# Kernel optimization log

Hardware: AMD Instinct MI355X
Metric: run time of the kernel (lower is better)

The kernel has to match this reference:

```python
import jax, jax.numpy as jnp
import numpy as np

B, S, D, H = 2, 2048, 1024, 16
HD = D // H
SCALE = HD ** -0.5


def setup_inputs() -> dict:
    key = jax.random.key(0)
    ks = jax.random.split(key, 11)
    std = D ** -0.5
    inp = {
        'query': jax.random.normal(ks[0], (B, S, D), jnp.float32),
        'key': jax.random.normal(ks[1], (B, S, D), jnp.float32),
        'value': jax.random.normal(ks[2], (B, S, D), jnp.float32),
        'Wq': jax.random.normal(ks[3], (D, D), jnp.float32) * std,
        'bq': jnp.zeros((D,), jnp.float32),
        'Wk': jax.random.normal(ks[4], (D, D), jnp.float32) * std,
        'bk': jnp.zeros((D,), jnp.float32),
        'Wv': jax.random.normal(ks[5], (D, D), jnp.float32) * std,
        'bv': jnp.zeros((D,), jnp.float32),
        'Wo': jax.random.normal(ks[6], (D, D), jnp.float32) * std,
        'bo': jnp.zeros((D,), jnp.float32),
    }
    return inp


def reference(query, key, value, Wq, bq, Wk, bk, Wv, bv, Wo, bo):
    # Linear projections (torch Linear: x @ W.T + b), split into heads -> [B,H,S,HD]
    def proj(x, W, b):
        y = jnp.einsum('bsd,ed->bse', x, W) + b
        return y.reshape(B, S, H, HD).transpose(0, 2, 1, 3)

    Q = proj(query, Wq, bq)
    K = proj(key, Wk, bk)
    V = proj(value, Wv, bv)
    scores = jnp.einsum('bhqd,bhkd->bhqk', Q, K) * SCALE  # [B,H,S,S]
    attn = jax.nn.softmax(scores, axis=-1)
    ctx = jnp.einsum('bhqk,bhkd->bhqd', attn, V)
    ctx = ctx.transpose(0, 2, 1, 3).reshape(B, S, D)
    out = jnp.einsum('bsd,ed->bse', ctx, Wo) + bo
    return out
```

## Files before the change

kernel.cpp:

```cpp
#include <hip/hip_runtime.h>
#include <hip/hip_bf16.h>

#define DEVFN __device__ __forceinline__

typedef __attribute__((ext_vector_type(8))) short bf16x8;
typedef __attribute__((ext_vector_type(4))) float f32x4;
typedef __attribute__((ext_vector_type(16))) float f32x16;

constexpr int Bc = 2, Sc = 2048, Dc = 1024, Hc = 16, HDc = 64;
constexpr float SCALEc = 0.125f;
constexpr float LOG2E  = 1.44269504088896340736f;

DEVFN unsigned short f2bf(float f) {
    union { float f; unsigned int u; } x; x.f = f;
    return (unsigned short)((x.u + 0x7fffu + ((x.u >> 16) & 1u)) >> 16);
}

DEVFN f32x4 mfma16(bf16x8 a, bf16x8 b, f32x4 c) {
    return __builtin_amdgcn_mfma_f32_16x16x32_bf16(a, b, c, 0, 0, 0);
}
DEVFN f32x16 mfma32(bf16x8 a, bf16x8 b, f32x16 c) {
    return __builtin_amdgcn_mfma_f32_32x32x16_bf16(a, b, c, 0, 0, 0);
}

DEVFN void gload16(const void* g, void* l) {
    __builtin_amdgcn_global_load_lds((const __attribute__((address_space(1))) void*)g,
                                     (__attribute__((address_space(3))) void*)l, 16, 0, 0);
}

__global__ __launch_bounds__(256) void cvt_all(
    const float* __restrict__ q, const float* __restrict__ k, const float* __restrict__ v,
    const float* __restrict__ wq, const float* __restrict__ wk,
    const float* __restrict__ wv, const float* __restrict__ wo,
    unsigned short* __restrict__ qb, unsigned short* __restrict__ kb, unsigned short* __restrict__ vb,
    unsigned short* __restrict__ wqb, unsigned short* __restrict__ wkb,
    unsigned short* __restrict__ wvb, unsigned short* __restrict__ wob)
{
    const unsigned t = blockIdx.x * 256 + threadIdx.x;
    const float* s; unsigned short* d; unsigned local;
    if (t < (3u << 19)) {
        const unsigned which = t >> 19; local = t & ((1u << 19) - 1);
        s = which == 0 ? q : which == 1 ? k : v;
        d = which == 0 ? qb : which == 1 ? kb : vb;
    } else {
        const unsigned t2 = t - (3u << 19);
        const unsigned which = t2 >> 17; local = t2 & ((1u << 17) - 1);
        s = which == 0 ? wq : which == 1 ? wk : which == 2 ? wv : wo;
        d = which == 0 ? wqb : which == 1 ? wkb : which == 2 ? wvb : wob;
    }
    const size_t off = (size_t)local * 8;
    float4 v0 = *(const float4*)(s + off);
    float4 v1 = *(const float4*)(s + off + 4);
    unsigned short t8[8] = {f2bf(v0.x), f2bf(v0.y), f2bf(v0.z), f2bf(v0.w),
                            f2bf(v1.x), f2bf(v1.y), f2bf(v1.z), f2bf(v1.w)};
    *(uint4*)(d + off) = *(const uint4*)t8;
}

__global__ __launch_bounds__(256) void qkv_gemm(
    const unsigned short* __restrict__ Aq, const unsigned short* __restrict__ Ak,
    const unsigned short* __restrict__ Av,
    const unsigned short* __restrict__ Wqb, const unsigned short* __restrict__ Wkb,
    const unsigned short* __restrict__ Wvb,
    const float* __restrict__ bqp, const float* __restrict__ bkp, const float* __restrict__ bvp,
    unsigned short* __restrict__ Qo, unsigned short* __restrict__ Ko, unsigned short* __restrict__ Vto)
{
    __shared__ short As[2][4096];
    __shared__ short Bs[2][4096];

    const int g = blockIdx.x >> 8;
    const unsigned short* A  = g == 0 ? Aq  : g == 1 ? Ak  : Av;
    const unsigned short* Bw = g == 0 ? Wqb : g == 1 ? Wkb : Wvb;
    const float* bias = g == 0 ? bqp : g == 1 ? bkp : bvp;
    const float scale = g == 0 ? SCALEc * LOG2E : 1.0f;

    const int tid = threadIdx.x, lane = tid & 63, w = tid >> 6;
    const int lr = lane & 15, lg = lane >> 4;
    const int bid = blockIdx.x & 255;
    const int tm = bid & 31, tn = bid >> 5;
    const int wm = (w >> 1) * 64, wn = (w & 1) * 64;

    const int c0 = 2 * w, c1 = 2 * w + 1;
    const int r0 = c0 * 16 + (lane >> 2), r1 = c1 * 16 + (lane >> 2);
    const int sl0 = ((lane & 3) ^ ((r0 >> 1) & 3)) * 8, sl1 = ((lane & 3) ^ ((r1 >> 1) & 3)) * 8;
    const unsigned short* Ap0 = A  + (size_t)(tm * 128 + r0) * 1024 + sl0;
    const unsigned short* Ap1 = A  + (size_t)(tm * 128 + r1) * 1024 + sl1;
    const unsigned short* Bp0 = Bw + (size_t)(tn * 128 + r0) * 1024 + sl0;
    const unsigned short* Bp1 = Bw + (size_t)(tn * 128 + r1) * 1024 + sl1;

    f32x4 acc[4][4] = {};
    const int fread = (lr >> 1) & 3;

    gload16(Ap0, &As[0][c0 * 512]);
    gload16(Ap1, &As[0][c1 * 512]);
    gload16(Bp0, &Bs[0][c0 * 512]);
    gload16(Bp1, &Bs[0][c1 * 512]);

    int cur = 0;
    for (int k0 = 0; k0 < 1024; k0 += 32) {
        const int nk = (k0 + 32 < 1024) ? k0 + 32 : k0;
        gload16(Ap0 + nk, &As[cur ^ 1][c0 * 512]);
        gload16(Ap1 + nk, &As[cur ^ 1][c1 * 512]);
        gload16(Bp0 + nk, &Bs[cur ^ 1][c0 * 512]);
        gload16(Bp1 + nk, &Bs[cur ^ 1][c1 * 512]);
        asm volatile("s_waitcnt vmcnt(4)" ::: "memory");
        __builtin_amdgcn_s_barrier();
        __builtin_amdgcn_sched_barrier(0);

        const short* Ac = As[cur];
        const short* Bc2 = Bs[cur];
        bf16x8 af[4], bfv[4];
        #pragma unroll
        for (int m = 0; m < 4; m++) {
            const int row = wm + m * 16 + lr;
            af[m] = *(const bf16x8*)&Ac[row * 32 + (lg ^ fread) * 8];
        }
        #pragma unroll
        for (int n = 0; n < 4; n++) {
            const int row = wn + n * 16 + lr;
            bfv[n] = *(const bf16x8*)&Bc2[row * 32 + (lg ^ fread) * 8];
        }
        #pragma unroll
        for (int m = 0; m < 4; m++)
            #pragma unroll
            for (int n = 0; n < 4; n++)
                acc[m][n] = mfma16(af[m], bfv[n], acc[m][n]);

        asm volatile("s_waitcnt lgkmcnt(0)" ::: "memory");
        __builtin_amdgcn_sched_barrier(0);
        __builtin_amdgcn_s_barrier();
        cur ^= 1;
    }
    asm volatile("s_waitcnt vmcnt(0)" ::: "memory");

    if (g < 2) {
        unsigned short* Y = g == 0 ? Qo : Ko;
        #pragma unroll
        for (int n = 0; n < 4; n++) {
            const int col = tn * 128 + wn + n * 16 + lr;
            const float bv = bias[col];
            const int hh = col >> 6, hd = col & 63;
            #pragma unroll
            for (int m = 0; m < 4; m++) {
                const int row0 = tm * 128 + wm + m * 16 + lg * 4;
                const int b_ = row0 >> 11, sQ = row0 & 2047;
                #pragma unroll
                for (int r = 0; r < 4; r++) {
                    const float val = (acc[m][n][r] + bv) * scale;
                    Y[(((size_t)(b_ * Hc + hh)) * Sc + (sQ + r)) * HDc + hd] = f2bf(val);
                }
            }
        }
    } else {
        #pragma unroll
        for (int n = 0; n < 4; n++) {
            const int col = tn * 128 + wn + n * 16 + lr;
            const float bv = bias[col];
            const int hh = col >> 6, hd = col & 63;
            #pragma unroll
            for (int m = 0; m < 4; m++) {
                const int row0 = tm * 128 + wm + m * 16 + lg * 4;
                const int b_ = row0 >> 11, sQ = row0 & 2047;
                const int sQp = (sQ & ~12) | ((sQ & 4) << 1) | ((sQ & 8) >> 1);
                unsigned long long pk = 0;
                #pragma unroll
                for (int r = 0; r < 4; r++)
                    pk |= (unsigned long long)f2bf(acc[m][n][r] + bv) << (16 * r);
                *(unsigned long long*)&Vto[(((size_t)(b_ * Hc + hh)) * HDc + hd) * Sc + sQp] = pk;
            }
        }
    }
}

__global__ __launch_bounds__(256) void out_gemm(
    const unsigned short* __restrict__ Ab, const unsigned short* __restrict__ Bw,
    const float* __restrict__ bias, float* __restrict__ Y)
{
    __shared__ short As[2][4096];
    __shared__ short Bs[2][4096];
    const int tid = threadIdx.x, lane = tid & 63, w = tid >> 6;
    const int lr = lane & 15, lg = lane >> 4;
    const int tm = blockIdx.x & 31, tn = blockIdx.x >> 5;
    const int wm = (w >> 1) * 64, wn = (w & 1) * 64;

    const int c0 = 2 * w, c1 = 2 * w + 1;
    const int r0 = c0 * 16 + (lane >> 2), r1 = c1 * 16 + (lane >> 2);
    const int sl0 = ((lane & 3) ^ ((r0 >> 1) & 3)) * 8, sl1 = ((lane & 3) ^ ((r1 >> 1) & 3)) * 8;
    const unsigned short* Ap0 = Ab + (size_t)(tm * 128 + r0) * 1024 + sl0;
    const unsigned short* Ap1 = Ab + (size_t)(tm * 128 + r1) * 1024 + sl1;
    const unsigned short* Bp0 = Bw + (size_t)(tn * 128 + r0) * 1024 + sl0;
    const unsigned short* Bp1 = Bw + (size_t)(tn * 128 + r1) * 1024 + sl1;

    f32x4 acc[4][4] = {};
    const int fread = (lr >> 1) & 3;

    gload16(Ap0, &As[0][c0 * 512]);
    gload16(Ap1, &As[0][c1 * 512]);
    gload16(Bp0, &Bs[0][c0 * 512]);
    gload16(Bp1, &Bs[0][c1 * 512]);

    int cur = 0;
    for (int k0 = 0; k0 < 1024; k0 += 32) {
        const int nk = (k0 + 32 < 1024) ? k0 + 32 : k0;
        gload16(Ap0 + nk, &As[cur ^ 1][c0 * 512]);
        gload16(Ap1 + nk, &As[cur ^ 1][c1 * 512]);
        gload16(Bp0 + nk, &Bs[cur ^ 1][c0 * 512]);
        gload16(Bp1 + nk, &Bs[cur ^ 1][c1 * 512]);
        asm volatile("s_waitcnt vmcnt(4)" ::: "memory");
        __builtin_amdgcn_s_barrier();
        __builtin_amdgcn_sched_barrier(0);

        const short* Ac = As[cur];
        const short* Bc2 = Bs[cur];
        bf16x8 af[4], bfv[4];
        #pragma unroll
        for (int m = 0; m < 4; m++) {
            const int row = wm + m * 16 + lr;
            af[m] = *(const bf16x8*)&Ac[row * 32 + (lg ^ fread) * 8];
        }
        #pragma unroll
        for (int n = 0; n < 4; n++) {
            const int row = wn + n * 16 + lr;
            bfv[n] = *(const bf16x8*)&Bc2[row * 32 + (lg ^ fread) * 8];
        }
        #pragma unroll
        for (int m = 0; m < 4; m++)
            #pragma unroll
            for (int n = 0; n < 4; n++)
                acc[m][n] = mfma16(af[m], bfv[n], acc[m][n]);

        asm volatile("s_waitcnt lgkmcnt(0)" ::: "memory");
        __builtin_amdgcn_sched_barrier(0);
        __builtin_amdgcn_s_barrier();
        cur ^= 1;
    }
    asm volatile("s_waitcnt vmcnt(0)" ::: "memory");

    #pragma unroll
    for (int n = 0; n < 4; n++) {
        const int col = tn * 128 + wn + n * 16 + lr;
        const float bv = bias[col];
        #pragma unroll
        for (int m = 0; m < 4; m++) {
            const int row0 = tm * 128 + wm + m * 16 + lg * 4;
            #pragma unroll
            for (int r = 0; r < 4; r++)
                Y[(size_t)(row0 + r) * 1024 + col] = acc[m][n][r] + bv;
        }
    }
}

__global__ __launch_bounds__(512, 2) void attn_fwd(
    const unsigned short* __restrict__ Q, const unsigned short* __restrict__ Kg,
    const unsigned short* __restrict__ Vtg, unsigned short* __restrict__ ctx)
{
    __shared__ short Ks[2][4096];
    __shared__ short Vs[2][4096];

    const int tid = threadIdx.x, lane = tid & 63, w = tid >> 6;
    const int l31 = lane & 31, hi = lane >> 5;

    const int blk = blockIdx.x;
    const int idx = blk >> 3;
    const int bh = (blk & 7) * 4 + (idx >> 3);
    const int qt = idx & 7;

    const unsigned short* Qb = Q   + (size_t)bh * Sc * HDc;
    const unsigned short* Kb = Kg  + (size_t)bh * Sc * HDc;
    const unsigned short* Vb = Vtg + (size_t)bh * HDc * Sc;

    const int qbase = qt * 256 + w * 32;
    bf16x8 qf[4];
    {
        const size_t qr = (size_t)(qbase + l31) * HDc + hi * 8;
        #pragma unroll
        for (int kk = 0; kk < 4; kk++)
            qf[kk] = *(const bf16x8*)&Qb[qr + kk * 16];
    }

    const int srow  = w * 8 + (lane >> 3);
    const int sslot = ((lane & 7) ^ (lane >> 3)) * 8;
    const unsigned short* Kst = Kb + (size_t)srow * HDc + sslot;
    const unsigned short* Vst = Vb + (size_t)srow * Sc + sslot;

    const int swk = lane & 7;

    const f32x16 Z = {};
    f32x16 acc0 = {}, acc1 = {}, accl = {};

    union { unsigned int u[4]; bf16x8 v; } ones;
    ones.u[0] = ones.u[1] = ones.u[2] = ones.u[3] = 0x3F803F80u;

    gload16(Kst, &Ks[0][w * 512]);
    gload16(Vst, &Vs[0][w * 512]);

    int cur = 0;
    for (int kt = 0; kt < 32; ++kt) {
        {
            const int nxt = kt < 31 ? kt + 1 : 31;
            gload16(Kst + (size_t)nxt * 4096, &Ks[cur ^ 1][w * 512]);
            gload16(Vst + nxt * 64,           &Vs[cur ^ 1][w * 512]);
        }
        asm volatile("s_waitcnt vmcnt(2)" ::: "memory");
        __builtin_amdgcn_s_barrier();
        __builtin_amdgcn_sched_barrier(0);

        const short* Kc = Ks[cur];
        const short* Vc = Vs[cur];

        f32x16 sf0, sf1;
        __builtin_amdgcn_s_setprio(1);
        {
            const int sl = (hi ^ swk) * 8;
            bf16x8 a0 = *(const bf16x8*)&Kc[l31 * 64 + sl];
            bf16x8 a1 = *(const bf16x8*)&Kc[(32 + l31) * 64 + sl];
            sf0 = mfma32(a0, qf[0], Z);
            sf1 = mfma32(a1, qf[0], Z);
        }
        #pragma unroll
        for (int kk = 1; kk < 4; kk++) {
            const int sl = ((2 * kk + hi) ^ swk) * 8;
            bf16x8 a0 = *(const bf16x8*)&Kc[l31 * 64 + sl];
            bf16x8 a1 = *(const bf16x8*)&Kc[(32 + l31) * 64 + sl];
            sf0 = mfma32(a0, qf[kk], sf0);
            sf1 = mfma32(a1, qf[kk], sf1);
        }
        __builtin_amdgcn_s_setprio(0);

        unsigned int p0[8], p1[8];
        #pragma unroll
        for (int j = 0; j < 8; j++) {
            const float a0 = __builtin_amdgcn_exp2f(sf0[2 * j]);
            const float a1 = __builtin_amdgcn_exp2f(sf0[2 * j + 1]);
            const float b0 = __builtin_amdgcn_exp2f(sf1[2 * j]);
            const float b1 = __builtin_amdgcn_exp2f(sf1[2 * j + 1]);
            asm("v_cvt_pk_bf16_f32 %0, %1, %2" : "=v"(p0[j]) : "v"(a0), "v"(a1));
            asm("v_cvt_pk_bf16_f32 %0, %1, %2" : "=v"(p1[j]) : "v"(b0), "v"(b1));
        }

        __builtin_amdgcn_s_setprio(1);
        #pragma unroll
        for (int m = 0; m < 4; m++) {
            const unsigned int* pw = (m < 2) ? &p0[(m & 1) * 4] : &p1[(m & 1) * 4];
            union { unsigned int u[4]; bf16x8 v; } af;
            af.u[0] = pw[0]; af.u[1] = pw[1]; af.u[2] = pw[2]; af.u[3] = pw[3];
            const int sl = ((2 * m + hi) ^ swk) * 8;
            bf16x8 b0 = *(const bf16x8*)&Vc[l31 * 64 + sl];
            bf16x8 b1 = *(const bf16x8*)&Vc[(32 + l31) * 64 + sl];
            acc0 = mfma32(af.v, b0, acc0);
            acc1 = mfma32(af.v, b1, acc1);
            accl = mfma32(af.v, ones.v, accl);
        }
        __builtin_amdgcn_s_setprio(0);

        asm volatile("s_waitcnt lgkmcnt(0)" ::: "memory");
        __builtin_amdgcn_sched_barrier(0);
        __builtin_amdgcn_s_barrier();
        cur ^= 1;
    }
    asm volatile("s_waitcnt vmcnt(0)" ::: "memory");

    const int b_ = bh >> 4, hh = bh & 15;
    #pragma unroll
    for (int r = 0; r < 16; r++) {
        const int qr = (r & 3) + 8 * (r >> 2) + 4 * hi;
        const float lv = __builtin_amdgcn_rcpf(accl[r]);
        const int sq = qbase + qr;
        unsigned short* co = &ctx[((size_t)(b_ * Sc + sq)) * Dc + (size_t)hh * HDc + l31];
        co[0]  = f2bf(acc0[r] * lv);
        co[32] = f2bf(acc1[r] * lv);
    }
}

extern "C" void kernel_launch(void* const* d_in, const int* in_sizes, int n_in,
                              void* d_out, int out_size, void* d_ws, size_t ws_size,
                              hipStream_t stream)
{
    const float* query = (const float*)d_in[0];
    const float* key   = (const float*)d_in[1];
    const float* value = (const float*)d_in[2];
    const float* Wq = (const float*)d_in[3];
    const float* bq = (const float*)d_in[4];
    const float* Wk = (const float*)d_in[5];
    const float* bk = (const float*)d_in[6];
    const float* Wv = (const float*)d_in[7];
    const float* bv = (const float*)d_in[8];
    const float* Wo = (const float*)d_in[9];
    const float* bo = (const float*)d_in[10];

    constexpr size_t W = 1048576, AE = 4194304;
    unsigned short* wqb = (unsigned short*)d_ws;
    unsigned short* wkb = wqb + W;
    unsigned short* wvb = wkb + W;
    unsigned short* wob = wvb + W;
    unsigned short* qb  = wob + W;
    unsigned short* kb  = qb + AE;
    unsigned short* vb  = kb + AE;
    unsigned short* Qh  = vb + AE;
    unsigned short* Kh  = Qh + AE;
    unsigned short* Vth = Kh + AE;
    unsigned short* cx  = qb;

    cvt_all<<<8192, 256, 0, stream>>>(query, key, value, Wq, Wk, Wv, Wo,
                                      qb, kb, vb, wqb, wkb, wvb, wob);
    qkv_gemm<<<768, 256, 0, stream>>>(qb, kb, vb, wqb, wkb, wvb,
                                      bq, bk, bv, Qh, Kh, Vth);
    attn_fwd<<<256, 512, 0, stream>>>(Qh, Kh, Vth, cx);
    out_gemm<<<256, 256, 0, stream>>>(cx, wob, bo, (float*)d_out);
}
```

Measured before the change: 131.0 us.

## Triple-buffer GEMM K-tiles and split attention into smaller 4-wave blocks

Both projection GEMMs move from double to triple-buffered LDS staging, prefetching two K-tiles ahead and waiting on vmcnt(8), so global load latency is better hidden behind MFMA work. The attention kernel goes from 256 blocks of 8 waves to 512 blocks of 4 waves. Each wave now loads twice as many K/V staging rows, and the block-to-(head, q-tile) mapping is adjusted to match. This adds LDS use per GEMM block and doubles per-block K/V load traffic in attention, in exchange for more deeply pipelined GEMMs and finer attention scheduling across CUs.

```diff
diff --git a/kernel.cpp b/kernel.cpp
--- a/kernel.cpp
+++ b/kernel.cpp
@@ -64,8 +64,8 @@
     const float* __restrict__ bqp, const float* __restrict__ bkp, const float* __restrict__ bvp,
     unsigned short* __restrict__ Qo, unsigned short* __restrict__ Ko, unsigned short* __restrict__ Vto)
 {
-    __shared__ short As[2][4096];
-    __shared__ short Bs[2][4096];
+    __shared__ short As[3 * 4096];
+    __shared__ short Bs[3 * 4096];
 
     const int g = blockIdx.x >> 8;
     const unsigned short* A  = g == 0 ? Aq  : g == 1 ? Ak  : Av;
@@ -90,24 +90,28 @@
     f32x4 acc[4][4] = {};
     const int fread = (lr >> 1) & 3;
 
-    gload16(Ap0, &As[0][c0 * 512]);
-    gload16(Ap1, &As[0][c1 * 512]);
-    gload16(Bp0, &Bs[0][c0 * 512]);
-    gload16(Bp1, &Bs[0][c1 * 512]);
-
-    int cur = 0;
+    gload16(Ap0,      As + 0    + c0 * 512);
+    gload16(Ap1,      As + 0    + c1 * 512);
+    gload16(Bp0,      Bs + 0    + c0 * 512);
+    gload16(Bp1,      Bs + 0    + c1 * 512);
+    gload16(Ap0 + 32, As + 4096 + c0 * 512);
+    gload16(Ap1 + 32, As + 4096 + c1 * 512);
+    gload16(Bp0 + 32, Bs + 4096 + c0 * 512);
+    gload16(Bp1 + 32, Bs + 4096 + c1 * 512);
+
+    int bR = 0, bN1 = 4096, bN2 = 8192;
     for (int k0 = 0; k0 < 1024; k0 += 32) {
-        const int nk = (k0 + 32 < 1024) ? k0 + 32 : k0;
-        gload16(Ap0 + nk, &As[cur ^ 1][c0 * 512]);
-        gload16(Ap1 + nk, &As[cur ^ 1][c1 * 512]);
-        gload16(Bp0 + nk, &Bs[cur ^ 1][c0 * 512]);
-        gload16(Bp1 + nk, &Bs[cur ^ 1][c1 * 512]);
-        asm volatile("s_waitcnt vmcnt(4)" ::: "memory");
-        __builtin_amdgcn_s_barrier();
-        __builtin_amdgcn_sched_barrier(0);
-
-        const short* Ac = As[cur];
-        const short* Bc2 = Bs[cur];
+        const int nk = (k0 + 64 < 1024) ? k0 + 64 : 992;
+        gload16(Ap0 + nk, As + bN2 + c0 * 512);
+        gload16(Ap1 + nk, As + bN2 + c1 * 512);
+        gload16(Bp0 + nk, Bs + bN2 + c0 * 512);
+        gload16(Bp1 + nk, Bs + bN2 + c1 * 512);
+        asm volatile("s_waitcnt vmcnt(8)" ::: "memory");
+        __builtin_amdgcn_s_barrier();
+        __builtin_amdgcn_sched_barrier(0);
+
+        const short* Ac  = As + bR;
+        const short* Bc2 = Bs + bR;
         bf16x8 af[4], bfv[4];
         #pragma unroll
         for (int m = 0; m < 4; m++) {
@@ -128,7 +132,7 @@
         asm volatile("s_waitcnt lgkmcnt(0)" ::: "memory");
         __builtin_amdgcn_sched_barrier(0);
         __builtin_amdgcn_s_barrier();
-        cur ^= 1;
+        const int t = bR; bR = bN1; bN1 = bN2; bN2 = t;
     }
     asm volatile("s_waitcnt vmcnt(0)" ::: "memory");
 
@@ -175,8 +179,8 @@
     const unsigned short* __restrict__ Ab, const unsigned short* __restrict__ Bw,
     const float* __restrict__ bias, float* __restrict__ Y)
 {
-    __shared__ short As[2][4096];
-    __shared__ short Bs[2][4096];
+    __shared__ short As[3 * 4096];
+    __shared__ short Bs[3 * 4096];
     const int tid = threadIdx.x, lane = tid & 63, w = tid >> 6;
     const int lr = lane & 15, lg = lane >> 4;
     const int tm = blockIdx.x & 31, tn = blockIdx.x >> 5;
@@ -193,24 +197,28 @@
     f32x4 acc[4][4] = {};
     const int fread = (lr >> 1) & 3;
 
-    gload16(Ap0, &As[0][c0 * 512]);
-    gload16(Ap1, &As[0][c1 * 512]);
-    gload16(Bp0, &Bs[0][c0 * 512]);
-    gload16(Bp1, &Bs[0][c1 * 512]);
-
-    int cur = 0;
+    gload16(Ap0,      As + 0    + c0 * 512);
+    gload16(Ap1,      As + 0    + c1 * 512);
+    gload16(Bp0,      Bs + 0    + c0 * 512);
+    gload16(Bp1,      Bs + 0    + c1 * 512);
+    gload16(Ap0 + 32, As + 4096 + c0 * 512);
+    gload16(Ap1 + 32, As + 4096 + c1 * 512);
+    gload16(Bp0 + 32, Bs + 4096 + c0 * 512);
+    gload16(Bp1 + 32, Bs + 4096 + c1 * 512);
+
+    int bR = 0, bN1 = 4096, bN2 = 8192;
     for (int k0 = 0; k0 < 1024; k0 += 32) {
-        const int nk = (k0 + 32 < 1024) ? k0 + 32 : k0;
-        gload16(Ap0 + nk, &As[cur ^ 1][c0 * 512]);
-        gload16(Ap1 + nk, &As[cur ^ 1][c1 * 512]);
-        gload16(Bp0 + nk, &Bs[cur ^ 1][c0 * 512]);
-        gload16(Bp1 + nk, &Bs[cur ^ 1][c1 * 512]);
-        asm volatile("s_waitcnt vmcnt(4)" ::: "memory");
-        __builtin_amdgcn_s_barrier();
-        __builtin_amdgcn_sched_barrier(0);
-
-        const short* Ac = As[cur];
-        const short* Bc2 = Bs[cur];
+        const int nk = (k0 + 64 < 1024) ? k0 + 64 : 992;
+        gload16(Ap0 + nk, As + bN2 + c0 * 512);
+        gload16(Ap1 + nk, As + bN2 + c1 * 512);
+        gload16(Bp0 + nk, Bs + bN2 + c0 * 512);
+        gload16(Bp1 + nk, Bs + bN2 + c1 * 512);
+        asm volatile("s_waitcnt vmcnt(8)" ::: "memory");
+        __builtin_amdgcn_s_barrier();
+        __builtin_amdgcn_sched_barrier(0);
+
+        const short* Ac  = As + bR;
+        const short* Bc2 = Bs + bR;
         bf16x8 af[4], bfv[4];
         #pragma unroll
         for (int m = 0; m < 4; m++) {
@@ -231,7 +239,7 @@
         asm volatile("s_waitcnt lgkmcnt(0)" ::: "memory");
         __builtin_amdgcn_sched_barrier(0);
         __builtin_amdgcn_s_barrier();
-        cur ^= 1;
+        const int t = bR; bR = bN1; bN1 = bN2; bN2 = t;
     }
     asm volatile("s_waitcnt vmcnt(0)" ::: "memory");
 
@@ -249,7 +257,7 @@
     }
 }
 
-__global__ __launch_bounds__(512, 2) void attn_fwd(
+__global__ __launch_bounds__(256) void attn_fwd(
     const unsigned short* __restrict__ Q, const unsigned short* __restrict__ Kg,
     const unsigned short* __restrict__ Vtg, unsigned short* __restrict__ ctx)
 {
@@ -261,14 +269,14 @@
 
     const int blk = blockIdx.x;
     const int idx = blk >> 3;
-    const int bh = (blk & 7) * 4 + (idx >> 3);
-    const int qt = idx & 7;
+    const int bh = (blk & 7) * 4 + (idx >> 4);
+    const int qt = idx & 15;
 
     const unsigned short* Qb = Q   + (size_t)bh * Sc * HDc;
     const unsigned short* Kb = Kg  + (size_t)bh * Sc * HDc;
     const unsigned short* Vb = Vtg + (size_t)bh * HDc * Sc;
 
-    const int qbase = qt * 256 + w * 32;
+    const int qbase = qt * 128 + w * 32;
     bf16x8 qf[4];
     {
         const size_t qr = (size_t)(qbase + l31) * HDc + hi * 8;
@@ -277,7 +285,7 @@
             qf[kk] = *(const bf16x8*)&Qb[qr + kk * 16];
     }
 
-    const int srow  = w * 8 + (lane >> 3);
+    const int srow  = w * 16 + (lane >> 3);
     const int sslot = ((lane & 7) ^ (lane >> 3)) * 8;
     const unsigned short* Kst = Kb + (size_t)srow * HDc + sslot;
     const unsigned short* Vst = Vb + (size_t)srow * Sc + sslot;
@@ -290,17 +298,25 @@
     union { unsigned int u[4]; bf16x8 v; } ones;
     ones.u[0] = ones.u[1] = ones.u[2] = ones.u[3] = 0x3F803F80u;
 
-    gload16(Kst, &Ks[0][w * 512]);
-    gload16(Vst, &Vs[0][w * 512]);
+    gload16(Kst,          &Ks[0][w * 1024]);
+    gload16(Kst + 512,    &Ks[0][w * 1024 + 512]);
+    gload16(Vst,          &Vs[0][w * 1024]);
+    gload16(Vst + 8 * Sc, &Vs[0][w * 1024 + 512]);
 
     int cur = 0;
     for (int kt = 0; kt < 32; ++kt) {
         {
             const int nxt = kt < 31 ? kt + 1 : 31;
-            gload16(Kst + (size_t)nxt * 4096, &Ks[cur ^ 1][w * 512]);
-            gload16(Vst + nxt * 64,           &Vs[cur ^ 1][w * 512]);
-        }
-        asm volatile("s_waitcnt vmcnt(2)" ::: "memory");
+            const unsigned short* kp = Kst + (size_t)nxt * 4096;
+            const unsigned short* vp = Vst + nxt * 64;
+            short* kl = &Ks[cur ^ 1][w * 1024];
+            short* vl = &Vs[cur ^ 1][w * 1024];
+            gload16(kp,           kl);
+            gload16(kp + 512,     kl + 512);
+            gload16(vp,           vl);
+            gload16(vp + 8 * Sc,  vl + 512);
+        }
+        asm volatile("s_waitcnt vmcnt(4)" ::: "memory");
         __builtin_amdgcn_s_barrier();
         __builtin_amdgcn_sched_barrier(0);
 
@@ -404,6 +420,6 @@
                                       qb, kb, vb, wqb, wkb, wvb, wob);
     qkv_gemm<<<768, 256, 0, stream>>>(qb, kb, vb, wqb, wkb, wvb,
                                       bq, bk, bv, Qh, Kh, Vth);
-    attn_fwd<<<256, 512, 0, stream>>>(Qh, Kh, Vth, cx);
+    attn_fwd<<<512, 256, 0, stream>>>(Qh, Kh, Vth, cx);
     out_gemm<<<256, 256, 0, stream>>>(cx, wob, bo, (float*)d_out);
 }
```

Result: slower. 136.2 us (+3.9%).

## Fuse fp32-to-bf16 activation conversion into QKV GEMM A-tile loads

Applied to the files above, without the earlier changes.

Stops the separate pass that converts query/key/value to bf16 into a workspace. The QKV GEMM now loads fp32 activation rows straight into registers two k-steps ahead, converts them with packed bf16 conversion instructions, and writes them into the swizzled LDS tile, while weights still arrive via direct global-to-LDS loads. This removes a full read/write round trip of the activations and part of a kernel launch. In exchange the GEMM reads twice the A bytes per tile, needs more registers for the in-flight loads (launch bounds set to 3 waves), and puts conversion ALU work inside the main loop.

```diff
diff --git a/kernel.cpp b/kernel.cpp
--- a/kernel.cpp
+++ b/kernel.cpp
@@ -28,26 +28,16 @@
                                      (__attribute__((address_space(3))) void*)l, 16, 0, 0);
 }
 
-__global__ __launch_bounds__(256) void cvt_all(
-    const float* __restrict__ q, const float* __restrict__ k, const float* __restrict__ v,
+__global__ __launch_bounds__(256) void cvt_w(
     const float* __restrict__ wq, const float* __restrict__ wk,
     const float* __restrict__ wv, const float* __restrict__ wo,
-    unsigned short* __restrict__ qb, unsigned short* __restrict__ kb, unsigned short* __restrict__ vb,
     unsigned short* __restrict__ wqb, unsigned short* __restrict__ wkb,
     unsigned short* __restrict__ wvb, unsigned short* __restrict__ wob)
 {
     const unsigned t = blockIdx.x * 256 + threadIdx.x;
-    const float* s; unsigned short* d; unsigned local;
-    if (t < (3u << 19)) {
-        const unsigned which = t >> 19; local = t & ((1u << 19) - 1);
-        s = which == 0 ? q : which == 1 ? k : v;
-        d = which == 0 ? qb : which == 1 ? kb : vb;
-    } else {
-        const unsigned t2 = t - (3u << 19);
-        const unsigned which = t2 >> 17; local = t2 & ((1u << 17) - 1);
-        s = which == 0 ? wq : which == 1 ? wk : which == 2 ? wv : wo;
-        d = which == 0 ? wqb : which == 1 ? wkb : which == 2 ? wvb : wob;
-    }
+    const unsigned which = t >> 17, local = t & ((1u << 17) - 1);
+    const float* s = which == 0 ? wq : which == 1 ? wk : which == 2 ? wv : wo;
+    unsigned short* d = which == 0 ? wqb : which == 1 ? wkb : which == 2 ? wvb : wob;
     const size_t off = (size_t)local * 8;
     float4 v0 = *(const float4*)(s + off);
     float4 v1 = *(const float4*)(s + off + 4);
@@ -56,9 +46,8 @@
     *(uint4*)(d + off) = *(const uint4*)t8;
 }
 
-__global__ __launch_bounds__(256) void qkv_gemm(
-    const unsigned short* __restrict__ Aq, const unsigned short* __restrict__ Ak,
-    const unsigned short* __restrict__ Av,
+__global__ __launch_bounds__(256, 3) void qkv_gemm(
+    const float* __restrict__ Aq, const float* __restrict__ Ak, const float* __restrict__ Av,
     const unsigned short* __restrict__ Wqb, const unsigned short* __restrict__ Wkb,
     const unsigned short* __restrict__ Wvb,
     const float* __restrict__ bqp, const float* __restrict__ bkp, const float* __restrict__ bvp,
@@ -68,7 +57,7 @@
     __shared__ short Bs[2][4096];
 
     const int g = blockIdx.x >> 8;
-    const unsigned short* A  = g == 0 ? Aq  : g == 1 ? Ak  : Av;
+    const float* A = g == 0 ? Aq : g == 1 ? Ak : Av;
     const unsigned short* Bw = g == 0 ? Wqb : g == 1 ? Wkb : Wvb;
     const float* bias = g == 0 ? bqp : g == 1 ? bkp : bvp;
     const float scale = g == 0 ? SCALEc * LOG2E : 1.0f;
@@ -81,56 +70,93 @@
 
     const int c0 = 2 * w, c1 = 2 * w + 1;
     const int r0 = c0 * 16 + (lane >> 2), r1 = c1 * 16 + (lane >> 2);
-    const int sl0 = ((lane & 3) ^ ((r0 >> 1) & 3)) * 8, sl1 = ((lane & 3) ^ ((r1 >> 1) & 3)) * 8;
-    const unsigned short* Ap0 = A  + (size_t)(tm * 128 + r0) * 1024 + sl0;
-    const unsigned short* Ap1 = A  + (size_t)(tm * 128 + r1) * 1024 + sl1;
-    const unsigned short* Bp0 = Bw + (size_t)(tn * 128 + r0) * 1024 + sl0;
-    const unsigned short* Bp1 = Bw + (size_t)(tn * 128 + r1) * 1024 + sl1;
+    const int s0 = (lane & 3) ^ ((r0 >> 1) & 3), s1 = (lane & 3) ^ ((r1 >> 1) & 3);
+    const float* Afp0 = A + (size_t)(tm * 128 + r0) * 1024 + s0 * 8;
+    const float* Afp1 = A + (size_t)(tm * 128 + r1) * 1024 + s1 * 8;
+    const unsigned short* Bp0 = Bw + (size_t)(tn * 128 + r0) * 1024 + s0 * 8;
+    const unsigned short* Bp1 = Bw + (size_t)(tn * 128 + r1) * 1024 + s1 * 8;
+    short* AW0[2] = {&As[0][c0 * 512 + lane * 8], &As[1][c0 * 512 + lane * 8]};
+    short* AW1[2] = {&As[0][c1 * 512 + lane * 8], &As[1][c1 * 512 + lane * 8]};
 
     f32x4 acc[4][4] = {};
     const int fread = (lr >> 1) & 3;
 
-    gload16(Ap0, &As[0][c0 * 512]);
-    gload16(Ap1, &As[0][c1 * 512]);
+    float4 fE[4], fO[4];
+
+    fE[0] = *(const float4*)(Afp0);     fE[1] = *(const float4*)(Afp0 + 4);
+    fE[2] = *(const float4*)(Afp1);     fE[3] = *(const float4*)(Afp1 + 4);
     gload16(Bp0, &Bs[0][c0 * 512]);
     gload16(Bp1, &Bs[0][c1 * 512]);
-
-    int cur = 0;
-    for (int k0 = 0; k0 < 1024; k0 += 32) {
-        const int nk = (k0 + 32 < 1024) ? k0 + 32 : k0;
-        gload16(Ap0 + nk, &As[cur ^ 1][c0 * 512]);
-        gload16(Ap1 + nk, &As[cur ^ 1][c1 * 512]);
-        gload16(Bp0 + nk, &Bs[cur ^ 1][c0 * 512]);
-        gload16(Bp1 + nk, &Bs[cur ^ 1][c1 * 512]);
-        asm volatile("s_waitcnt vmcnt(4)" ::: "memory");
-        __builtin_amdgcn_s_barrier();
-        __builtin_amdgcn_sched_barrier(0);
-
-        const short* Ac = As[cur];
-        const short* Bc2 = Bs[cur];
-        bf16x8 af[4], bfv[4];
-        #pragma unroll
-        for (int m = 0; m < 4; m++) {
-            const int row = wm + m * 16 + lr;
-            af[m] = *(const bf16x8*)&Ac[row * 32 + (lg ^ fread) * 8];
-        }
-        #pragma unroll
-        for (int n = 0; n < 4; n++) {
-            const int row = wn + n * 16 + lr;
-            bfv[n] = *(const bf16x8*)&Bc2[row * 32 + (lg ^ fread) * 8];
-        }
-        #pragma unroll
-        for (int m = 0; m < 4; m++)
-            #pragma unroll
-            for (int n = 0; n < 4; n++)
-                acc[m][n] = mfma16(af[m], bfv[n], acc[m][n]);
-
-        asm volatile("s_waitcnt lgkmcnt(0)" ::: "memory");
-        __builtin_amdgcn_sched_barrier(0);
-        __builtin_amdgcn_s_barrier();
-        cur ^= 1;
+    {
+        unsigned int q0, q1, q2, q3;
+        asm("v_cvt_pk_bf16_f32 %0,%1,%2" : "=v"(q0) : "v"(fE[0].x), "v"(fE[0].y));
+        asm("v_cvt_pk_bf16_f32 %0,%1,%2" : "=v"(q1) : "v"(fE[0].z), "v"(fE[0].w));
+        asm("v_cvt_pk_bf16_f32 %0,%1,%2" : "=v"(q2) : "v"(fE[1].x), "v"(fE[1].y));
+        asm("v_cvt_pk_bf16_f32 %0,%1,%2" : "=v"(q3) : "v"(fE[1].z), "v"(fE[1].w));
+        *(uint4*)AW0[0] = (uint4){q0, q1, q2, q3};
+        asm("v_cvt_pk_bf16_f32 %0,%1,%2" : "=v"(q0) : "v"(fE[2].x), "v"(fE[2].y));
+        asm("v_cvt_pk_bf16_f32 %0,%1,%2" : "=v"(q1) : "v"(fE[2].z), "v"(fE[2].w));
+        asm("v_cvt_pk_bf16_f32 %0,%1,%2" : "=v"(q2) : "v"(fE[3].x), "v"(fE[3].y));
+        asm("v_cvt_pk_bf16_f32 %0,%1,%2" : "=v"(q3) : "v"(fE[3].z), "v"(fE[3].w));
+        *(uint4*)AW1[0] = (uint4){q0, q1, q2, q3};
+    }
+    fO[0] = *(const float4*)(Afp0 + 32); fO[1] = *(const float4*)(Afp0 + 36);
+    fO[2] = *(const float4*)(Afp1 + 32); fO[3] = *(const float4*)(Afp1 + 36);
+    asm volatile("s_waitcnt lgkmcnt(0)" ::: "memory");
+
+#define QKV_STEP(KT, P, FI, FC)                                                  \
+    {                                                                            \
+        const int k1 = ((KT) < 31) ? ((KT) + 1) * 32 : 992;                      \
+        const int k2 = ((KT) < 30) ? ((KT) + 2) * 32 : 992;                      \
+        gload16(Bp0 + k1, &Bs[(P) ^ 1][c0 * 512]);                               \
+        gload16(Bp1 + k1, &Bs[(P) ^ 1][c1 * 512]);                               \
+        FI[0] = *(const float4*)(Afp0 + k2); FI[1] = *(const float4*)(Afp0 + k2 + 4); \
+        FI[2] = *(const float4*)(Afp1 + k2); FI[3] = *(const float4*)(Afp1 + k2 + 4); \
+        asm volatile("s_waitcnt vmcnt(10)" ::: "memory");                        \
+        __builtin_amdgcn_s_barrier();                                            \
+        __builtin_amdgcn_sched_barrier(0);                                       \
+        const short* Ac  = As[P];                                                \
+        const short* Bc2 = Bs[P];                                                \
+        bf16x8 af[4], bfv[4];                                                    \
+        _Pragma("unroll")                                                        \
+        for (int m = 0; m < 4; m++) {                                            \
+            const int row = wm + m * 16 + lr;                                    \
+            af[m] = *(const bf16x8*)&Ac[row * 32 + (lg ^ fread) * 8];            \
+        }                                                                        \
+        _Pragma("unroll")                                                        \
+        for (int n = 0; n < 4; n++) {                                            \
+            const int row = wn + n * 16 + lr;                                    \
+            bfv[n] = *(const bf16x8*)&Bc2[row * 32 + (lg ^ fread) * 8];          \
+        }                                                                        \
+        _Pragma("unroll")                                                        \
+        for (int m = 0; m < 4; m++)                                              \
+            _Pragma("unroll")                                                    \
+            for (int n = 0; n < 4; n++)                                          \
+                acc[m][n] = mfma16(af[m], bfv[n], acc[m][n]);                    \
+        {                                                                        \
+            unsigned int q0, q1, q2, q3;                                         \
+            asm("v_cvt_pk_bf16_f32 %0,%1,%2" : "=v"(q0) : "v"(FC[0].x), "v"(FC[0].y)); \
+            asm("v_cvt_pk_bf16_f32 %0,%1,%2" : "=v"(q1) : "v"(FC[0].z), "v"(FC[0].w)); \
+            asm("v_cvt_pk_bf16_f32 %0,%1,%2" : "=v"(q2) : "v"(FC[1].x), "v"(FC[1].y)); \
+            asm("v_cvt_pk_bf16_f32 %0,%1,%2" : "=v"(q3) : "v"(FC[1].z), "v"(FC[1].w)); \
+            *(uint4*)AW0[(P) ^ 1] = (uint4){q0, q1, q2, q3};                     \
+            asm("v_cvt_pk_bf16_f32 %0,%1,%2" : "=v"(q0) : "v"(FC[2].x), "v"(FC[2].y)); \
+            asm("v_cvt_pk_bf16_f32 %0,%1,%2" : "=v"(q1) : "v"(FC[2].z), "v"(FC[2].w)); \
+            asm("v_cvt_pk_bf16_f32 %0,%1,%2" : "=v"(q2) : "v"(FC[3].x), "v"(FC[3].y)); \
+            asm("v_cvt_pk_bf16_f32 %0,%1,%2" : "=v"(q3) : "v"(FC[3].z), "v"(FC[3].w)); \
+            *(uint4*)AW1[(P) ^ 1] = (uint4){q0, q1, q2, q3};                     \
+        }                                                                        \
+        asm volatile("s_waitcnt lgkmcnt(0)" ::: "memory");                       \
+        __builtin_amdgcn_sched_barrier(0);                                       \
+        __builtin_amdgcn_s_barrier();                                            \
+    }
+
+    for (int kt = 0; kt < 32; kt += 2) {
+        QKV_STEP(kt,     0, fE, fO)
+        QKV_STEP(kt + 1, 1, fO, fE)
     }
     asm volatile("s_waitcnt vmcnt(0)" ::: "memory");
+#undef QKV_STEP
 
     if (g < 2) {
         unsigned short* Y = g == 0 ? Qo : Ko;
@@ -209,7 +235,7 @@
         __builtin_amdgcn_s_barrier();
         __builtin_amdgcn_sched_barrier(0);
 
-        const short* Ac = As[cur];
+        const short* Ac  = As[cur];
         const short* Bc2 = Bs[cur];
         bf16x8 af[4], bfv[4];
         #pragma unroll
@@ -392,17 +418,13 @@
     unsigned short* wkb = wqb + W;
     unsigned short* wvb = wkb + W;
     unsigned short* wob = wvb + W;
-    unsigned short* qb  = wob + W;
-    unsigned short* kb  = qb + AE;
-    unsigned short* vb  = kb + AE;
-    unsigned short* Qh  = vb + AE;
+    unsigned short* Qh  = wob + W;
     unsigned short* Kh  = Qh + AE;
     unsigned short* Vth = Kh + AE;
-    unsigned short* cx  = qb;
-
-    cvt_all<<<8192, 256, 0, stream>>>(query, key, value, Wq, Wk, Wv, Wo,
-                                      qb, kb, vb, wqb, wkb, wvb, wob);
-    qkv_gemm<<<768, 256, 0, stream>>>(qb, kb, vb, wqb, wkb, wvb,
+    unsigned short* cx  = Vth + AE;
+
+    cvt_w<<<2048, 256, 0, stream>>>(Wq, Wk, Wv, Wo, wqb, wkb, wvb, wob);
+    qkv_gemm<<<768, 256, 0, stream>>>(query, key, value, wqb, wkb, wvb,
                                       bq, bk, bv, Qh, Kh, Vth);
     attn_fwd<<<256, 512, 0, stream>>>(Qh, Kh, Vth, cx);
     out_gemm<<<256, 256, 0, stream>>>(cx, wob, bo, (float*)d_out);
```

Measured after the change: 115.5 us. 11.8% less time.

## Fuse fp32-to-bf16 activation conversion into QKV GEMM with larger tiles

Applied to the files above, without the earlier changes.

The separate conversion pass over query/key/value is removed. The QKV GEMM now loads fp32 activations directly, converts them in registers with packed bf16 conversion instructions, and writes them into swizzled LDS. The GEMM also moves to 256x256 tiles with 512 threads, a BK of 64, an XCD-aware block remap and raised wave priority around the MFMA section. This avoids writing and re-reading about 24MB of bf16 activations, in exchange for more fp32 global traffic inside the GEMM and only 192 blocks, which may underfill the device.

```diff
diff --git a/kernel.cpp b/kernel.cpp
--- a/kernel.cpp
+++ b/kernel.cpp
@@ -28,26 +28,16 @@
                                      (__attribute__((address_space(3))) void*)l, 16, 0, 0);
 }
 
-__global__ __launch_bounds__(256) void cvt_all(
-    const float* __restrict__ q, const float* __restrict__ k, const float* __restrict__ v,
+__global__ __launch_bounds__(256) void cvt_w(
     const float* __restrict__ wq, const float* __restrict__ wk,
     const float* __restrict__ wv, const float* __restrict__ wo,
-    unsigned short* __restrict__ qb, unsigned short* __restrict__ kb, unsigned short* __restrict__ vb,
     unsigned short* __restrict__ wqb, unsigned short* __restrict__ wkb,
     unsigned short* __restrict__ wvb, unsigned short* __restrict__ wob)
 {
     const unsigned t = blockIdx.x * 256 + threadIdx.x;
-    const float* s; unsigned short* d; unsigned local;
-    if (t < (3u << 19)) {
-        const unsigned which = t >> 19; local = t & ((1u << 19) - 1);
-        s = which == 0 ? q : which == 1 ? k : v;
-        d = which == 0 ? qb : which == 1 ? kb : vb;
-    } else {
-        const unsigned t2 = t - (3u << 19);
-        const unsigned which = t2 >> 17; local = t2 & ((1u << 17) - 1);
-        s = which == 0 ? wq : which == 1 ? wk : which == 2 ? wv : wo;
-        d = which == 0 ? wqb : which == 1 ? wkb : which == 2 ? wvb : wob;
-    }
+    const unsigned which = t >> 17, local = t & ((1u << 17) - 1);
+    const float* s = which == 0 ? wq : which == 1 ? wk : which == 2 ? wv : wo;
+    unsigned short* d = which == 0 ? wqb : which == 1 ? wkb : which == 2 ? wvb : wob;
     const size_t off = (size_t)local * 8;
     float4 v0 = *(const float4*)(s + off);
     float4 v1 = *(const float4*)(s + off + 4);
@@ -56,34 +46,187 @@
     *(uint4*)(d + off) = *(const uint4*)t8;
 }
 
-__global__ __launch_bounds__(256) void qkv_gemm(
-    const unsigned short* __restrict__ Aq, const unsigned short* __restrict__ Ak,
-    const unsigned short* __restrict__ Av,
+__global__ __launch_bounds__(512, 2) void qkv_gemm(
+    const float* __restrict__ Aq, const float* __restrict__ Ak, const float* __restrict__ Av,
     const unsigned short* __restrict__ Wqb, const unsigned short* __restrict__ Wkb,
     const unsigned short* __restrict__ Wvb,
     const float* __restrict__ bqp, const float* __restrict__ bkp, const float* __restrict__ bvp,
     unsigned short* __restrict__ Qo, unsigned short* __restrict__ Ko, unsigned short* __restrict__ Vto)
 {
-    __shared__ short As[2][4096];
-    __shared__ short Bs[2][4096];
-
-    const int g = blockIdx.x >> 8;
-    const unsigned short* A  = g == 0 ? Aq  : g == 1 ? Ak  : Av;
+    __shared__ short As[2 * 16384];
+    __shared__ short Bs[2 * 16384];
+
+    const int lgid = (blockIdx.x & 7) * 24 + (blockIdx.x >> 3);
+    const int g = lgid >> 6;
+    const int rr = lgid & 63;
+    const int tm = rr >> 2, tn = rr & 3;
+
+    const float* A = g == 0 ? Aq : g == 1 ? Ak : Av;
     const unsigned short* Bw = g == 0 ? Wqb : g == 1 ? Wkb : Wvb;
     const float* bias = g == 0 ? bqp : g == 1 ? bkp : bvp;
     const float scale = g == 0 ? SCALEc * LOG2E : 1.0f;
 
     const int tid = threadIdx.x, lane = tid & 63, w = tid >> 6;
+    const int lr = lane & 15, lgq = lane >> 4;
+    const int wm = (w >> 2) * 128, wn = (w & 3) * 64;
+
+    const int ra = tid >> 1, kh = tid & 1;
+    const int swzra = (ra & 7) ^ (((ra >> 3) & 1) << 2);
+    const float* Ap = A + (size_t)(tm * 256 + ra) * 1024 + kh * 32;
+    const int aw0 = ra * 64 + (((kh * 4 + 0) ^ swzra) * 8);
+    const int aw1 = ra * 64 + (((kh * 4 + 1) ^ swzra) * 8);
+    const int aw2 = ra * 64 + (((kh * 4 + 2) ^ swzra) * 8);
+    const int aw3 = ra * 64 + (((kh * 4 + 3) ^ swzra) * 8);
+
+    const int l3 = lane >> 3, l7 = lane & 7;
+    const unsigned short* Bp[4];
+    #pragma unroll
+    for (int i = 0; i < 4; i++) {
+        const int rb = w * 32 + i * 8 + l3;
+        const int swzrb = (rb & 7) ^ (((rb >> 3) & 1) << 2);
+        Bp[i] = Bw + (size_t)(tn * 256 + rb) * 1024 + ((l7 ^ swzrb) * 8);
+    }
+    const int bdst = (w * 32) * 64;
+
+    const int swzL = (lr & 7) ^ (((lr >> 3) & 1) << 2);
+
+    f32x4 acc[8][4] = {};
+    float4 fA0, fA1, fA2, fA3, fA4, fA5, fA6, fA7;
+
+#define LOAD_A(KO)                                                               \
+    fA0 = *(const float4*)(Ap + (KO));      fA1 = *(const float4*)(Ap + (KO) + 4);  \
+    fA2 = *(const float4*)(Ap + (KO) + 8);  fA3 = *(const float4*)(Ap + (KO) + 12); \
+    fA4 = *(const float4*)(Ap + (KO) + 16); fA5 = *(const float4*)(Ap + (KO) + 20); \
+    fA6 = *(const float4*)(Ap + (KO) + 24); fA7 = *(const float4*)(Ap + (KO) + 28);
+
+#define CVT_A(BUFOFS)                                                            \
+    {                                                                            \
+        unsigned int q0, q1, q2, q3;                                             \
+        asm("v_cvt_pk_bf16_f32 %0,%1,%2" : "=v"(q0) : "v"(fA0.x), "v"(fA0.y));   \
+        asm("v_cvt_pk_bf16_f32 %0,%1,%2" : "=v"(q1) : "v"(fA0.z), "v"(fA0.w));   \
+        asm("v_cvt_pk_bf16_f32 %0,%1,%2" : "=v"(q2) : "v"(fA1.x), "v"(fA1.y));   \
+        asm("v_cvt_pk_bf16_f32 %0,%1,%2" : "=v"(q3) : "v"(fA1.z), "v"(fA1.w));   \
+        *(uint4*)&As[(BUFOFS) + aw0] = (uint4){q0, q1, q2, q3};                  \
+        asm("v_cvt_pk_bf16_f32 %0,%1,%2" : "=v"(q0) : "v"(fA2.x), "v"(fA2.y));   \
+        asm("v_cvt_pk_bf16_f32 %0,%1,%2" : "=v"(q1) : "v"(fA2.z), "v"(fA2.w));   \
+        asm("v_cvt_pk_bf16_f32 %0,%1,%2" : "=v"(q2) : "v"(fA3.x), "v"(fA3.y));   \
+        asm("v_cvt_pk_bf16_f32 %0,%1,%2" : "=v"(q3) : "v"(fA3.z), "v"(fA3.w));   \
+        *(uint4*)&As[(BUFOFS) + aw1] = (uint4){q0, q1, q2, q3};                  \
+        asm("v_cvt_pk_bf16_f32 %0,%1,%2" : "=v"(q0) : "v"(fA4.x), "v"(fA4.y));   \
+        asm("v_cvt_pk_bf16_f32 %0,%1,%2" : "=v"(q1) : "v"(fA4.z), "v"(fA4.w));   \
+        asm("v_cvt_pk_bf16_f32 %0,%1,%2" : "=v"(q2) : "v"(fA5.x), "v"(fA5.y));   \
+        asm("v_cvt_pk_bf16_f32 %0,%1,%2" : "=v"(q3) : "v"(fA5.z), "v"(fA5.w));   \
+        *(uint4*)&As[(BUFOFS) + aw2] = (uint4){q0, q1, q2, q3};                  \
+        asm("v_cvt_pk_bf16_f32 %0,%1,%2" : "=v"(q0) : "v"(fA6.x), "v"(fA6.y));   \
+        asm("v_cvt_pk_bf16_f32 %0,%1,%2" : "=v"(q1) : "v"(fA6.z), "v"(fA6.w));   \
+        asm("v_cvt_pk_bf16_f32 %0,%1,%2" : "=v"(q2) : "v"(fA7.x), "v"(fA7.y));   \
+        asm("v_cvt_pk_bf16_f32 %0,%1,%2" : "=v"(q3) : "v"(fA7.z), "v"(fA7.w));   \
+        *(uint4*)&As[(BUFOFS) + aw3] = (uint4){q0, q1, q2, q3};                  \
+    }
+
+    gload16(Bp[0], &Bs[bdst + 0]);
+    gload16(Bp[1], &Bs[bdst + 512]);
+    gload16(Bp[2], &Bs[bdst + 1024]);
+    gload16(Bp[3], &Bs[bdst + 1536]);
+    LOAD_A(0)
+    CVT_A(0)
+    asm volatile("s_waitcnt vmcnt(0) lgkmcnt(0)" ::: "memory");
+    __builtin_amdgcn_s_barrier();
+
+    for (int t = 0; t < 16; ++t) {
+        const int Pofs = (t & 1) * 16384;
+        const int Nofs = Pofs ^ 16384;
+        if (t < 15) {
+            const int ko = (t + 1) * 64;
+            gload16(Bp[0] + ko, &Bs[Nofs + bdst + 0]);
+            gload16(Bp[1] + ko, &Bs[Nofs + bdst + 512]);
+            gload16(Bp[2] + ko, &Bs[Nofs + bdst + 1024]);
+            gload16(Bp[3] + ko, &Bs[Nofs + bdst + 1536]);
+            LOAD_A(ko)
+        }
+
+        __builtin_amdgcn_s_setprio(1);
+        #pragma unroll
+        for (int kh2 = 0; kh2 < 2; kh2++) {
+            const int sA = ((lgq + kh2 * 4) ^ swzL) * 8;
+            bf16x8 af[8], bf[4];
+            #pragma unroll
+            for (int m = 0; m < 8; m++)
+                af[m] = *(const bf16x8*)&As[Pofs + (wm + m * 16 + lr) * 64 + sA];
+            #pragma unroll
+            for (int n = 0; n < 4; n++)
+                bf[n] = *(const bf16x8*)&Bs[Pofs + (wn + n * 16 + lr) * 64 + sA];
+            #pragma unroll
+            for (int m = 0; m < 8; m++)
+                #pragma unroll
+                for (int n = 0; n < 4; n++)
+                    acc[m][n] = mfma16(af[m], bf[n], acc[m][n]);
+        }
+        __builtin_amdgcn_s_setprio(0);
+
+        if (t < 15) { CVT_A(Nofs) }
+        asm volatile("s_waitcnt lgkmcnt(0)" ::: "memory");
+        __builtin_amdgcn_sched_barrier(0);
+        __builtin_amdgcn_s_barrier();
+    }
+#undef LOAD_A
+#undef CVT_A
+
+    if (g < 2) {
+        unsigned short* Y = g == 0 ? Qo : Ko;
+        #pragma unroll
+        for (int n = 0; n < 4; n++) {
+            const int col = tn * 256 + wn + n * 16 + lr;
+            const float bv = bias[col];
+            const int hh = col >> 6, hd = col & 63;
+            #pragma unroll
+            for (int m = 0; m < 8; m++) {
+                const int row0 = tm * 256 + wm + m * 16 + lgq * 4;
+                const int b_ = row0 >> 11, sQ = row0 & 2047;
+                #pragma unroll
+                for (int r = 0; r < 4; r++) {
+                    const float val = (acc[m][n][r] + bv) * scale;
+                    Y[(((size_t)(b_ * Hc + hh)) * Sc + (sQ + r)) * HDc + hd] = f2bf(val);
+                }
+            }
+        }
+    } else {
+        #pragma unroll
+        for (int n = 0; n < 4; n++) {
+            const int col = tn * 256 + wn + n * 16 + lr;
+            const float bv = bias[col];
+            const int hh = col >> 6, hd = col & 63;
+            #pragma unroll
+            for (int m = 0; m < 8; m++) {
+                const int row0 = tm * 256 + wm + m * 16 + lgq * 4;
+                const int b_ = row0 >> 11, sQ = row0 & 2047;
+                const int sQp = (sQ & ~12) | ((sQ & 4) << 1) | ((sQ & 8) >> 1);
+                unsigned long long pk = 0;
+                #pragma unroll
+                for (int r = 0; r < 4; r++)
+                    pk |= (unsigned long long)f2bf(acc[m][n][r] + bv) << (16 * r);
+                *(unsigned long long*)&Vto[(((size_t)(b_ * Hc + hh)) * HDc + hd) * Sc + sQp] = pk;
+            }
+        }
+    }
+}
+
+__global__ __launch_bounds__(256) void out_gemm(
+    const unsigned short* __restrict__ Ab, const unsigned short* __restrict__ Bw,
+    const float* __restrict__ bias, float* __restrict__ Y)
+{
+    __shared__ short As[2][4096];
+    __shared__ short Bs[2][4096];
+    const int tid = threadIdx.x, lane = tid & 63, w = tid >> 6;
     const int lr = lane & 15, lg = lane >> 4;
-    const int bid = blockIdx.x & 255;
-    const int tm = bid & 31, tn = bid >> 5;
+    const int tm = blockIdx.x & 31, tn = blockIdx.x >> 5;
     const int wm = (w >> 1) * 64, wn = (w & 1) * 64;
 
     const int c0 = 2 * w, c1 = 2 * w + 1;
     const int r0 = c0 * 16 + (lane >> 2), r1 = c1 * 16 + (lane >> 2);
     const int sl0 = ((lane & 3) ^ ((r0 >> 1) & 3)) * 8, sl1 = ((lane & 3) ^ ((r1 >> 1) & 3)) * 8;
-    const unsigned short* Ap0 = A  + (size_t)(tm * 128 + r0) * 1024 + sl0;
-    const unsigned short* Ap1 = A  + (size_t)(tm * 128 + r1) * 1024 + sl1;
+    const unsigned short* Ap0 = Ab + (size_t)(tm * 128 + r0) * 1024 + sl0;
+    const unsigned short* Ap1 = Ab + (size_t)(tm * 128 + r1) * 1024 + sl1;
     const unsigned short* Bp0 = Bw + (size_t)(tn * 128 + r0) * 1024 + sl0;
     const unsigned short* Bp1 = Bw + (size_t)(tn * 128 + r1) * 1024 + sl1;
 
@@ -106,110 +249,7 @@
         __builtin_amdgcn_s_barrier();
         __builtin_amdgcn_sched_barrier(0);
 
-        const short* Ac = As[cur];
-        const short* Bc2 = Bs[cur];
-        bf16x8 af[4], bfv[4];
-        #pragma unroll
-        for (int m = 0; m < 4; m++) {
-            const int row = wm + m * 16 + lr;
-            af[m] = *(const bf16x8*)&Ac[row * 32 + (lg ^ fread) * 8];
-        }
-        #pragma unroll
-        for (int n = 0; n < 4; n++) {
-            const int row = wn + n * 16 + lr;
-            bfv[n] = *(const bf16x8*)&Bc2[row * 32 + (lg ^ fread) * 8];
-        }
-        #pragma unroll
-        for (int m = 0; m < 4; m++)
-            #pragma unroll
-            for (int n = 0; n < 4; n++)
-                acc[m][n] = mfma16(af[m], bfv[n], acc[m][n]);
-
-        asm volatile("s_waitcnt lgkmcnt(0)" ::: "memory");
-        __builtin_amdgcn_sched_barrier(0);
-        __builtin_amdgcn_s_barrier();
-        cur ^= 1;
-    }
-    asm volatile("s_waitcnt vmcnt(0)" ::: "memory");
-
-    if (g < 2) {
-        unsigned short* Y = g == 0 ? Qo : Ko;
-        #pragma unroll
-        for (int n = 0; n < 4; n++) {
-            const int col = tn * 128 + wn + n * 16 + lr;
-            const float bv = bias[col];
-            const int hh = col >> 6, hd = col & 63;
-            #pragma unroll
-            for (int m = 0; m < 4; m++) {
-                const int row0 = tm * 128 + wm + m * 16 + lg * 4;
-                const int b_ = row0 >> 11, sQ = row0 & 2047;
-                #pragma unroll
-                for (int r = 0; r < 4; r++) {
-                    const float val = (acc[m][n][r] + bv) * scale;
-                    Y[(((size_t)(b_ * Hc + hh)) * Sc + (sQ + r)) * HDc + hd] = f2bf(val);
-                }
-            }
-        }
-    } else {
-        #pragma unroll
-        for (int n = 0; n < 4; n++) {
-            const int col = tn * 128 + wn + n * 16 + lr;
-            const float bv = bias[col];
-            const int hh = col >> 6, hd = col & 63;
-            #pragma unroll
-            for (int m = 0; m < 4; m++) {
-                const int row0 = tm * 128 + wm + m * 16 + lg * 4;
-                const int b_ = row0 >> 11, sQ = row0 & 2047;
-                const int sQp = (sQ & ~12) | ((sQ & 4) << 1) | ((sQ & 8) >> 1);
-                unsigned long long pk = 0;
-                #pragma unroll
-                for (int r = 0; r < 4; r++)
-                    pk |= (unsigned long long)f2bf(acc[m][n][r] + bv) << (16 * r);
-                *(unsigned long long*)&Vto[(((size_t)(b_ * Hc + hh)) * HDc + hd) * Sc + sQp] = pk;
-            }
-        }
-    }
-}
-
-__global__ __launch_bounds__(256) void out_gemm(
-    const unsigned short* __restrict__ Ab, const unsigned short* __restrict__ Bw,
-    const float* __restrict__ bias, float* __restrict__ Y)
-{
-    __shared__ short As[2][4096];
-    __shared__ short Bs[2][4096];
-    const int tid = threadIdx.x, lane = tid & 63, w = tid >> 6;
-    const int lr = lane & 15, lg = lane >> 4;
-    const int tm = blockIdx.x & 31, tn = blockIdx.x >> 5;
-    const int wm = (w >> 1) * 64, wn = (w & 1) * 64;
-
-    const int c0 = 2 * w, c1 = 2 * w + 1;
-    const int r0 = c0 * 16 + (lane >> 2), r1 = c1 * 16 + (lane >> 2);
-    const int sl0 = ((lane & 3) ^ ((r0 >> 1) & 3)) * 8, sl1 = ((lane & 3) ^ ((r1 >> 1) & 3)) * 8;
-    const unsigned short* Ap0 = Ab + (size_t)(tm * 128 + r0) * 1024 + sl0;
-    const unsigned short* Ap1 = Ab + (size_t)(tm * 128 + r1) * 1024 + sl1;
-    const unsigned short* Bp0 = Bw + (size_t)(tn * 128 + r0) * 1024 + sl0;
-    const unsigned short* Bp1 = Bw + (size_t)(tn * 128 + r1) * 1024 + sl1;
-
-    f32x4 acc[4][4] = {};
-    const int fread = (lr >> 1) & 3;
-
-    gload16(Ap0, &As[0][c0 * 512]);
-    gload16(Ap1, &As[0][c1 * 512]);
-    gload16(Bp0, &Bs[0][c0 * 512]);
-    gload16(Bp1, &Bs[0][c1 * 512]);
-
-    int cur = 0;
-    for (int k0 = 0; k0 < 1024; k0 += 32) {
-        const int nk = (k0 + 32 < 1024) ? k0 + 32 : k0;
-        gload16(Ap0 + nk, &As[cur ^ 1][c0 * 512]);
-        gload16(Ap1 + nk, &As[cur ^ 1][c1 * 512]);
-        gload16(Bp0 + nk, &Bs[cur ^ 1][c0 * 512]);
-        gload16(Bp1 + nk, &Bs[cur ^ 1][c1 * 512]);
-        asm volatile("s_waitcnt vmcnt(4)" ::: "memory");
-        __builtin_amdgcn_s_barrier();
-        __builtin_amdgcn_sched_barrier(0);
-
-        const short* Ac = As[cur];
+        const short* Ac  = As[cur];
         const short* Bc2 = Bs[cur];
         bf16x8 af[4], bfv[4];
         #pragma unroll
@@ -392,17 +432,13 @@
     unsigned short* wkb = wqb + W;
     unsigned short* wvb = wkb + W;
     unsigned short* wob = wvb + W;
-    unsigned short* qb  = wob + W;
-    unsigned short* kb  = qb + AE;
-    unsigned short* vb  = kb + AE;
-    unsigned short* Qh  = vb + AE;
+    unsigned short* Qh  = wob + W;
     unsigned short* Kh  = Qh + AE;
     unsigned short* Vth = Kh + AE;
-    unsigned short* cx  = qb;
-
-    cvt_all<<<8192, 256, 0, stream>>>(query, key, value, Wq, Wk, Wv, Wo,
-                                      qb, kb, vb, wqb, wkb, wvb, wob);
-    qkv_gemm<<<768, 256, 0, stream>>>(qb, kb, vb, wqb, wkb, wvb,
+    unsigned short* cx  = Vth + AE;
+
+    cvt_w<<<2048, 256, 0, stream>>>(Wq, Wk, Wv, Wo, wqb, wkb, wvb, wob);
+    qkv_gemm<<<192, 512, 0, stream>>>(query, key, value, wqb, wkb, wvb,
                                       bq, bk, bv, Qh, Kh, Vth);
     attn_fwd<<<256, 512, 0, stream>>>(Qh, Kh, Vth, cx);
     out_gemm<<<256, 256, 0, stream>>>(cx, wob, bo, (float*)d_out);
```

Result: slower. 140.7 us (+7.4%).
